# Performance work log

Measured on AMD Instinct MI355X. Metric: run time of the kernel, lower is better.

Reference implementation:

```python
import jax, jax.numpy as jnp
import numpy as np

L, H, P = 16384, 1024, 512
DT_MIN, DT_MAX = 1e-3, 1e-1
STEP_RESCALE = 1.0


def setup_inputs() -> dict:
    key = jax.random.key(0)
    ks = jax.random.split(key, 7)
    input_sequence = jax.random.normal(ks[0], (L, H), jnp.float32)
    # eigenvalues with negative real part (left half plane), HiPPO-like imag parts
    Lambda_re = -(jax.random.uniform(ks[1], (P,), jnp.float32) * 0.9 + 0.1)
    Lambda_im = jnp.pi * jnp.arange(P, dtype=jnp.float32)
    B = jax.random.normal(ks[2], (P, H, 2), jnp.float32) / jnp.sqrt(2.0 * H)   # real/imag of B_tilde (P,H)
    C = jax.random.normal(ks[3], (H, P, 2), jnp.float32) / jnp.sqrt(2.0 * P)   # real/imag of C_tilde (H,P)
    D = jax.random.normal(ks[4], (H,), jnp.float32)
    u01 = jax.random.uniform(ks[5], (P, 1), jnp.float32)
    log_step = jnp.log(DT_MIN) + u01 * (jnp.log(DT_MAX) - jnp.log(DT_MIN))     # (P,1)
    return dict(input_sequence=input_sequence, Lambda_re=Lambda_re, Lambda_im=Lambda_im,
                B=B, C=C, D=D, log_step=log_step)


def _binop(q_i, q_j):
    # diagonal linear recurrence composition: (A, b) pairs
    A_i, b_i = q_i
    A_j, b_j = q_j
    return A_j * A_i, A_j * b_i + b_j


def reference(input_sequence, Lambda_re, Lambda_im, B, C, D, log_step):
    Lambda = Lambda_re + 1j * Lambda_im                        # (P,) complex64
    B_tilde = B[..., 0] + 1j * B[..., 1]                       # (P,H)
    C_tilde = C[..., 0] + 1j * C[..., 1]                       # (H,P)
    step = STEP_RESCALE * jnp.exp(log_step[:, 0])              # (P,)
    # ZOH discretization
    Lambda_bar = jnp.exp(Lambda * step)                        # (P,)
    B_bar = ((Lambda_bar - 1.0) / Lambda)[:, None] * B_tilde   # (P,H)
    # Bu_elements: (L,P) complex
    Bu = input_sequence.astype(B_bar.dtype) @ B_bar.T
    Lambda_elems = jnp.broadcast_to(Lambda_bar, Bu.shape)      # (L,P)
    # parallel associative scan over the diagonal recurrence x_t = Lambda_bar*x_{t-1} + Bu_t
    _, xs = jax.lax.associative_scan(_binop, (Lambda_elems, Bu))
    ys = 2.0 * (xs @ C_tilde.T).real                           # conj_sym => factor 2, (L,H)
    return ys + D * input_sequence
```

## Files before the change

kernel.cpp:

```cpp
#include <hip/hip_runtime.h>
#include <math.h>

#define L_SEQ 16384
#define H_DIM 1024
#define P_DIM 512
#define N2P   1024
#define KDIM  1024
#define NKT   16
#define CHUNK 64
#define NCHUNK 256

typedef __attribute__((ext_vector_type(8))) short short8;
typedef __attribute__((ext_vector_type(4))) float f32x4;
typedef __attribute__((address_space(3))) const char* lds3_t;

__device__ __forceinline__ unsigned short f2bf(float f){
    unsigned int u = __float_as_uint(f);
    u = (u + 0x7FFFu + ((u >> 16) & 1u)) >> 16;
    return (unsigned short)u;
}
__device__ __forceinline__ float bf2f(unsigned int lo16){
    return __uint_as_float(lo16 << 16);
}

__global__ void k_prep_lambda(const float* __restrict__ lre, const float* __restrict__ lim,
                              const float* __restrict__ lstep,
                              float* __restrict__ lam, float* __restrict__ coef,
                              float* __restrict__ lpow)
{
    int p = threadIdx.x;
    double step = exp((double)lstep[p]);
    double dr = (double)lre[p], di = (double)lim[p];
    double ar = dr*step, ai = di*step;
    double er = exp(ar);
    double lbr = er*cos(ai), lbi = er*sin(ai);
    lam[2*p] = (float)lbr; lam[2*p+1] = (float)lbi;
    double nr = lbr - 1.0, ni = lbi;
    double d2 = dr*dr + di*di;
    coef[2*p]   = (float)((nr*dr + ni*di)/d2);
    coef[2*p+1] = (float)((ni*dr - nr*di)/d2);
    double xr = lbr, xi = lbi;
    #pragma unroll
    for (int s=0;s<6;s++){ double t = xr*xr - xi*xi; xi = 2.0*xr*xi; xr = t; }
    lpow[2*p] = (float)xr; lpow[2*p+1] = (float)xi;
}

__global__ __launch_bounds__(256)
void k_prep_BB(const float* __restrict__ B, const float* __restrict__ coef,
               unsigned short* __restrict__ BB)
{
    int i = blockIdx.x*256 + threadIdx.x;
    int p = i >> 10, h = i & 1023;
    float br = B[2*i], bi = B[2*i+1];
    float cr = coef[2*p], ci = coef[2*p+1];
    BB[(size_t)(2*p)*H_DIM + h]   = f2bf(cr*br - ci*bi);
    BB[(size_t)(2*p+1)*H_DIM + h] = f2bf(cr*bi + ci*br);
}

__global__ __launch_bounds__(256)
void k_prep_CC(const float* __restrict__ C, unsigned short* __restrict__ CC)
{
    int i = blockIdx.x*256 + threadIdx.x;
    int h = i >> 9, p = i & 511;
    float cr = C[2*i], ci = C[2*i+1];
    CC[(size_t)h*N2P + 2*p]     = f2bf(2.f*cr);
    CC[(size_t)h*N2P + 2*p + 1] = f2bf(-2.f*ci);
}

__global__ __launch_bounds__(256)
void k_cast(const float4* __restrict__ u, unsigned short* __restrict__ o)
{
    int i = blockIdx.x*256 + threadIdx.x;
    float4 a = u[2*i], b = u[2*i+1];
    union { short8 v; unsigned short s[8]; } r;
    r.s[0]=f2bf(a.x); r.s[1]=f2bf(a.y); r.s[2]=f2bf(a.z); r.s[3]=f2bf(a.w);
    r.s[4]=f2bf(b.x); r.s[5]=f2bf(b.y); r.s[6]=f2bf(b.z); r.s[7]=f2bf(b.w);
    *reinterpret_cast<short8*>(o + (size_t)i*8) = r.v;
}

template<int EPI>
__global__ __launch_bounds__(512, 2)
void gemm256(const unsigned short* __restrict__ A, const unsigned short* __restrict__ Bm,
             float* __restrict__ Cf, unsigned short* __restrict__ Cb,
             const float* __restrict__ Dv, const unsigned short* __restrict__ U16)
{
    __shared__ char lds[131072];
    const int tid  = threadIdx.x;
    const int lane = tid & 63;
    const int wid  = tid >> 6;
    const int wm = wid >> 2, wn = wid & 3;
    const int wg = ((int)blockIdx.x & 7) * 32 + ((int)blockIdx.x >> 3);
    const int tm = wg >> 2, tn = wg & 3;
    const int lr = lane & 15;

    const int scol = ((tid & 7) ^ ((tid >> 3) & 7)) << 3;
    const int srow = tid >> 3;
    const int kc0 = (((lane >> 4)      ^ (lr & 7)) << 4);
    const int kc1 = ((((lane >> 4) | 4) ^ (lr & 7)) << 4);
    const int aSub = wm*16384 + lr*128;
    const int bSub = 32768 + (wn >> 1)*16384 + (wn & 1)*8192 + lr*128;

#define GLOAD(SRC, DST) __builtin_amdgcn_global_load_lds( \
        (const __attribute__((address_space(1))) void*)(SRC), \
        (__attribute__((address_space(3))) void*)(DST), 16, 0, 0)
#define STAGE_A(kt_, h_) do{ \
    char* d_ = lds + (((kt_)&1)<<16) + (h_)*16384 + tid*16; \
    const unsigned short* s_ = A + (size_t)(tm*256 + (h_)*128 + srow)*KDIM + (size_t)(kt_)*64 + scol; \
    GLOAD(s_, d_); GLOAD(s_ + (size_t)64*KDIM, d_ + 8192); }while(0)
#define STAGE_B(kt_, h_) do{ \
    char* d_ = lds + (((kt_)&1)<<16) + 32768 + (h_)*16384 + tid*16; \
    const unsigned short* s_ = Bm + (size_t)(tn*256 + (h_)*128 + srow)*KDIM + (size_t)(kt_)*64 + scol; \
    GLOAD(s_, d_); GLOAD(s_ + (size_t)64*KDIM, d_ + 8192); }while(0)
#define DSR(D, P, IMM) asm volatile("ds_read_b128 %0, %1 offset:" IMM : "=v"(D) : "v"(P))
#define LGKM(N) do{ asm volatile("s_waitcnt lgkmcnt(" #N ")" ::: "memory"); \
                    __builtin_amdgcn_sched_barrier(0); }while(0)
#define VMC4  asm volatile("s_waitcnt vmcnt(4)" ::: "memory")
#define ABAR  asm volatile("s_barrier" ::: "memory")
#define SB0   __builtin_amdgcn_sched_barrier(0)
#define MFMA(a,b,c) __builtin_amdgcn_mfma_f32_16x16x32_bf16(a,b,c,0,0,0)
#define PRIO1 __builtin_amdgcn_s_setprio(1)
#define PRIO0 __builtin_amdgcn_s_setprio(0)

    short8 a1[4], a2[4], bb0[4], bb1[4];
    f32x4 acc[8][4];
    #pragma unroll
    for (int m=0;m<8;m++)
        #pragma unroll
        for (int n=0;n<4;n++) acc[m][n] = (f32x4){0.f,0.f,0.f,0.f};

    STAGE_A(0,0); STAGE_A(0,1); STAGE_B(0,0); STAGE_B(0,1); STAGE_B(1,0); STAGE_B(1,1);
    VMC4; ABAR;

    #pragma unroll 2
    for (int kt = 0; kt < NKT; ++kt) {
        const int sb = (kt & 1) << 16;
        const int tA = (kt+1 < NKT) ? kt+1 : NKT-1;
        const int tB = (kt+2 < NKT) ? kt+2 : NKT-1;
        lds3_t pa0 = (lds3_t)(lds + sb + aSub + kc0);
        lds3_t pa1 = (lds3_t)(lds + sb + aSub + kc1);
        lds3_t pb0 = (lds3_t)(lds + sb + bSub + kc0);
        lds3_t pb1 = (lds3_t)(lds + sb + bSub + kc1);

        DSR(a1[0], pa0, "0");    DSR(a1[1], pa0, "2048");
        DSR(a1[2], pa0, "4096"); DSR(a1[3], pa0, "6144");
        DSR(bb0[0], pb0, "0");    DSR(bb0[1], pb0, "2048");
        DSR(bb0[2], pb0, "4096"); DSR(bb0[3], pb0, "6144");
        STAGE_A(tA, 0); STAGE_A(tA, 1);
        DSR(a2[0], pa0, "8192");  DSR(a2[1], pa0, "10240");
        DSR(a2[2], pa0, "12288"); DSR(a2[3], pa0, "14336");
        LGKM(4);
        PRIO1;
        #pragma unroll
        for (int m=0;m<4;m++)
            #pragma unroll
            for (int n=0;n<4;n++) acc[m][n] = MFMA(a1[m], bb0[n], acc[m][n]);
        PRIO0; SB0;
        DSR(a1[0], pa1, "0");    DSR(a1[1], pa1, "2048");
        DSR(a1[2], pa1, "4096"); DSR(a1[3], pa1, "6144");
        DSR(bb1[0], pb1, "0");    DSR(bb1[1], pb1, "2048");
        DSR(bb1[2], pb1, "4096"); DSR(bb1[3], pb1, "6144");
        LGKM(8);
        PRIO1;
        #pragma unroll
        for (int m=0;m<4;m++)
            #pragma unroll
            for (int n=0;n<4;n++) acc[4+m][n] = MFMA(a2[m], bb0[n], acc[4+m][n]);
        PRIO0; SB0;
        DSR(a2[0], pa1, "8192");  DSR(a2[1], pa1, "10240");
        DSR(a2[2], pa1, "12288"); DSR(a2[3], pa1, "14336");
        LGKM(4);
        ABAR;
        STAGE_B(tB, 0); STAGE_B(tB, 1);
        PRIO1;
        #pragma unroll
        for (int m=0;m<4;m++)
            #pragma unroll
            for (int n=0;n<4;n++) acc[m][n] = MFMA(a1[m], bb1[n], acc[m][n]);
        PRIO0; SB0;
        LGKM(0);
        PRIO1;
        #pragma unroll
        for (int m=0;m<4;m++)
            #pragma unroll
            for (int n=0;n<4;n++) acc[4+m][n] = MFMA(a2[m], bb1[n], acc[4+m][n]);
        PRIO0; SB0;
        VMC4;
        ABAR;
    }
    asm volatile("s_waitcnt vmcnt(0)" ::: "memory");

    const int orow0 = tm*256 + wm*128 + (lane>>4)*4;
    const int ocol0 = tn*256 + wn*64 + lr;
    #pragma unroll
    for (int m=0;m<8;m++){
        #pragma unroll
        for (int n=0;n<4;n++){
            int row = orow0 + m*16, col = ocol0 + n*16;
            #pragma unroll
            for (int j=0;j<4;j++){
                size_t idx = (size_t)(row + j)*N2P + col;
                if (EPI) Cf[idx] = acc[m][n][j] + Dv[col]*bf2f(U16[idx]);
                else     Cb[idx] = f2bf(acc[m][n][j]);
            }
        }
    }
#undef GLOAD
#undef STAGE_A
#undef STAGE_B
#undef DSR
#undef LGKM
#undef VMC4
#undef ABAR
#undef SB0
#undef MFMA
#undef PRIO1
#undef PRIO0
}

__global__ __launch_bounds__(512)
void k_agg(const unsigned int* __restrict__ Bu, const float* __restrict__ lam,
           float* __restrict__ agg)
{
    int p = threadIdx.x, c = blockIdx.x;
    float lrr = lam[2*p], lii = lam[2*p+1];
    float xr = 0.f, xi = 0.f;
    const unsigned int* b2 = Bu + (size_t)c*CHUNK*512 + p;
    #pragma unroll 4
    for (int t=0;t<CHUNK;t++){
        unsigned int b = b2[(size_t)t*512];
        float br = __uint_as_float(b << 16);
        float bi = __uint_as_float(b & 0xffff0000u);
        float tr = lrr*xr - lii*xi + br;
        xi = lrr*xi + lii*xr + bi;
        xr = tr;
    }
    agg[((size_t)c*P_DIM + p)*2]     = xr;
    agg[((size_t)c*P_DIM + p)*2 + 1] = xi;
}

__global__ __launch_bounds__(256)
void k_scan(const float* __restrict__ agg, const float* __restrict__ lpow,
            float* __restrict__ xinit)
{
    __shared__ float sr[NCHUNK], si[NCHUNK];
    int c = threadIdx.x, p = blockIdx.x;
    float xr = agg[((size_t)c*P_DIM + p)*2];
    float xi = agg[((size_t)c*P_DIM + p)*2 + 1];
    sr[c] = xr; si[c] = xi;
    float wr = lpow[2*p], wi = lpow[2*p+1];
    for (int s=1; s<NCHUNK; s<<=1){
        __syncthreads();
        float ur = 0.f, ui = 0.f;
        if (c >= s){ ur = sr[c-s]; ui = si[c-s]; }
        __syncthreads();
        xr += wr*ur - wi*ui;
        xi += wr*ui + wi*ur;
        sr[c] = xr; si[c] = xi;
        float t = wr*wr - wi*wi; wi = 2.f*wr*wi; wr = t;
    }
    __syncthreads();
    float er = 0.f, ei = 0.f;
    if (c > 0){ er = sr[c-1]; ei = si[c-1]; }
    xinit[((size_t)c*P_DIM + p)*2]     = er;
    xinit[((size_t)c*P_DIM + p)*2 + 1] = ei;
}

__global__ __launch_bounds__(512)
void k_apply(const unsigned int* __restrict__ Bu, const float* __restrict__ lam,
             const float* __restrict__ xinit, unsigned int* __restrict__ xs)
{
    int p = threadIdx.x, c = blockIdx.x;
    float lrr = lam[2*p], lii = lam[2*p+1];
    float xr = xinit[((size_t)c*P_DIM + p)*2];
    float xi = xinit[((size_t)c*P_DIM + p)*2 + 1];
    const unsigned int* b2 = Bu + (size_t)c*CHUNK*512 + p;
    unsigned int* o = xs + (size_t)c*CHUNK*512 + p;
    #pragma unroll 4
    for (int t=0;t<CHUNK;t++){
        unsigned int b = b2[(size_t)t*512];
        float br = __uint_as_float(b << 16);
        float bi = __uint_as_float(b & 0xffff0000u);
        float tr = lrr*xr - lii*xi + br;
        xi = lrr*xi + lii*xr + bi;
        xr = tr;
        o[(size_t)t*512] = (unsigned int)f2bf(xr) | ((unsigned int)f2bf(xi) << 16);
    }
}

extern "C" void kernel_launch(void* const* d_in, const int* in_sizes, int n_in,
                              void* d_out, int out_size, void* d_ws, size_t ws_size,
                              hipStream_t stream)
{
    const float* u   = (const float*)d_in[0];
    const float* lre = (const float*)d_in[1];
    const float* lim = (const float*)d_in[2];
    const float* B   = (const float*)d_in[3];
    const float* C   = (const float*)d_in[4];
    const float* D   = (const float*)d_in[5];
    const float* ls  = (const float*)d_in[6];
    float* out = (float*)d_out;

    char* w = (char*)d_ws;
    unsigned short* u16  = (unsigned short*)(w + 0);
    unsigned short* xs16 = (unsigned short*)(w + 33554432);
    unsigned short* Bu16 = (unsigned short*)(w + 67108864);
    unsigned short* BB   = (unsigned short*)(w + 100663296);
    unsigned short* CC   = (unsigned short*)(w + 102760448);
    float* lam   = (float*)(w + 104857600);
    float* coef  = (float*)(w + 104861696);
    float* lpow  = (float*)(w + 104865792);
    float* agg   = (float*)(w + 104869888);
    float* xinit = (float*)(w + 105918464);

    k_prep_lambda<<<1, P_DIM, 0, stream>>>(lre, lim, ls, lam, coef, lpow);
    k_prep_BB<<<(P_DIM*H_DIM)/256, 256, 0, stream>>>(B, coef, BB);
    k_prep_CC<<<(H_DIM*P_DIM)/256, 256, 0, stream>>>(C, CC);
    k_cast<<<(L_SEQ*H_DIM)/(256*8), 256, 0, stream>>>((const float4*)u, u16);

    gemm256<0><<<256, 512, 0, stream>>>(u16, BB, nullptr, Bu16, nullptr, nullptr);

    k_agg<<<NCHUNK, P_DIM, 0, stream>>>((const unsigned int*)Bu16, lam, agg);
    k_scan<<<P_DIM, NCHUNK, 0, stream>>>(agg, lpow, xinit);
    k_apply<<<NCHUNK, P_DIM, 0, stream>>>((const unsigned int*)Bu16, lam, xinit,
                                          (unsigned int*)xs16);

    gemm256<1><<<256, 512, 0, stream>>>(xs16, CC, out, nullptr, D, u16);
}
```

Measured before the change: 129.0 us.

## Replace hand-scheduled asm GEMM main loop with simple compiler-scheduled double buffer

The bf16 MFMA GEMM main loop drops its hand-written ds_read_b128 asm, explicit lgkmcnt waits, sched barriers and s_setprio. It also drops the staggered prefetch in which the next A tile and the B tile two steps ahead were staged mid-iteration. Now A and B for the next k-tile are both issued at the top of each iteration, fragments are read with plain LDS loads, and each iteration ends with a full vmcnt(0) wait and a barrier. The code is simpler and leaves scheduling to the compiler, but it gives up the fine-grained overlap of LDS reads, global-to-LDS copies and MFMA issue, and adds a full memory drain each iteration.

```diff
diff --git a/kernel.cpp b/kernel.cpp
--- a/kernel.cpp
+++ b/kernel.cpp
@@ -12,7 +12,6 @@
 
 typedef __attribute__((ext_vector_type(8))) short short8;
 typedef __attribute__((ext_vector_type(4))) float f32x4;
-typedef __attribute__((address_space(3))) const char* lds3_t;
 
 __device__ __forceinline__ unsigned short f2bf(float f){
     unsigned int u = __float_as_uint(f);
@@ -111,83 +110,47 @@
     char* d_ = lds + (((kt_)&1)<<16) + 32768 + (h_)*16384 + tid*16; \
     const unsigned short* s_ = Bm + (size_t)(tn*256 + (h_)*128 + srow)*KDIM + (size_t)(kt_)*64 + scol; \
     GLOAD(s_, d_); GLOAD(s_ + (size_t)64*KDIM, d_ + 8192); }while(0)
-#define DSR(D, P, IMM) asm volatile("ds_read_b128 %0, %1 offset:" IMM : "=v"(D) : "v"(P))
-#define LGKM(N) do{ asm volatile("s_waitcnt lgkmcnt(" #N ")" ::: "memory"); \
-                    __builtin_amdgcn_sched_barrier(0); }while(0)
-#define VMC4  asm volatile("s_waitcnt vmcnt(4)" ::: "memory")
+#define RD(OFF) (*(const short8*)(lds + (OFF)))
+#define MFMA(a,b,c) __builtin_amdgcn_mfma_f32_16x16x32_bf16(a,b,c,0,0,0)
+#define VMC0  asm volatile("s_waitcnt vmcnt(0)" ::: "memory")
 #define ABAR  asm volatile("s_barrier" ::: "memory")
-#define SB0   __builtin_amdgcn_sched_barrier(0)
-#define MFMA(a,b,c) __builtin_amdgcn_mfma_f32_16x16x32_bf16(a,b,c,0,0,0)
-#define PRIO1 __builtin_amdgcn_s_setprio(1)
-#define PRIO0 __builtin_amdgcn_s_setprio(0)
-
-    short8 a1[4], a2[4], bb0[4], bb1[4];
+
     f32x4 acc[8][4];
     #pragma unroll
     for (int m=0;m<8;m++)
         #pragma unroll
         for (int n=0;n<4;n++) acc[m][n] = (f32x4){0.f,0.f,0.f,0.f};
 
-    STAGE_A(0,0); STAGE_A(0,1); STAGE_B(0,0); STAGE_B(0,1); STAGE_B(1,0); STAGE_B(1,1);
-    VMC4; ABAR;
+    STAGE_A(0,0); STAGE_A(0,1); STAGE_B(0,0); STAGE_B(0,1);
+    VMC0; ABAR;
 
     #pragma unroll 2
     for (int kt = 0; kt < NKT; ++kt) {
         const int sb = (kt & 1) << 16;
-        const int tA = (kt+1 < NKT) ? kt+1 : NKT-1;
-        const int tB = (kt+2 < NKT) ? kt+2 : NKT-1;
-        lds3_t pa0 = (lds3_t)(lds + sb + aSub + kc0);
-        lds3_t pa1 = (lds3_t)(lds + sb + aSub + kc1);
-        lds3_t pb0 = (lds3_t)(lds + sb + bSub + kc0);
-        lds3_t pb1 = (lds3_t)(lds + sb + bSub + kc1);
-
-        DSR(a1[0], pa0, "0");    DSR(a1[1], pa0, "2048");
-        DSR(a1[2], pa0, "4096"); DSR(a1[3], pa0, "6144");
-        DSR(bb0[0], pb0, "0");    DSR(bb0[1], pb0, "2048");
-        DSR(bb0[2], pb0, "4096"); DSR(bb0[3], pb0, "6144");
-        STAGE_A(tA, 0); STAGE_A(tA, 1);
-        DSR(a2[0], pa0, "8192");  DSR(a2[1], pa0, "10240");
-        DSR(a2[2], pa0, "12288"); DSR(a2[3], pa0, "14336");
-        LGKM(4);
-        PRIO1;
+        const int tN = (kt+1 < NKT) ? kt+1 : NKT-1;
+        STAGE_A(tN, 0); STAGE_A(tN, 1); STAGE_B(tN, 0); STAGE_B(tN, 1);
+
         #pragma unroll
-        for (int m=0;m<4;m++)
+        for (int ks=0; ks<2; ++ks){
+            const int kc = ks ? kc1 : kc0;
+            short8 bfr[4];
             #pragma unroll
-            for (int n=0;n<4;n++) acc[m][n] = MFMA(a1[m], bb0[n], acc[m][n]);
-        PRIO0; SB0;
-        DSR(a1[0], pa1, "0");    DSR(a1[1], pa1, "2048");
-        DSR(a1[2], pa1, "4096"); DSR(a1[3], pa1, "6144");
-        DSR(bb1[0], pb1, "0");    DSR(bb1[1], pb1, "2048");
-        DSR(bb1[2], pb1, "4096"); DSR(bb1[3], pb1, "6144");
-        LGKM(8);
-        PRIO1;
-        #pragma unroll
-        for (int m=0;m<4;m++)
+            for (int n=0;n<4;n++) bfr[n] = RD(sb + bSub + n*2048 + kc);
             #pragma unroll
-            for (int n=0;n<4;n++) acc[4+m][n] = MFMA(a2[m], bb0[n], acc[4+m][n]);
-        PRIO0; SB0;
-        DSR(a2[0], pa1, "8192");  DSR(a2[1], pa1, "10240");
-        DSR(a2[2], pa1, "12288"); DSR(a2[3], pa1, "14336");
-        LGKM(4);
+            for (int mh=0; mh<2; ++mh){
+                short8 afr[4];
+                #pragma unroll
+                for (int m=0;m<4;m++) afr[m] = RD(sb + aSub + (mh*4+m)*2048 + kc);
+                #pragma unroll
+                for (int m=0;m<4;m++)
+                    #pragma unroll
+                    for (int n=0;n<4;n++)
+                        acc[mh*4+m][n] = MFMA(afr[m], bfr[n], acc[mh*4+m][n]);
+            }
+        }
+        VMC0;
         ABAR;
-        STAGE_B(tB, 0); STAGE_B(tB, 1);
-        PRIO1;
-        #pragma unroll
-        for (int m=0;m<4;m++)
-            #pragma unroll
-            for (int n=0;n<4;n++) acc[m][n] = MFMA(a1[m], bb1[n], acc[m][n]);
-        PRIO0; SB0;
-        LGKM(0);
-        PRIO1;
-        #pragma unroll
-        for (int m=0;m<4;m++)
-            #pragma unroll
-            for (int n=0;n<4;n++) acc[4+m][n] = MFMA(a2[m], bb1[n], acc[4+m][n]);
-        PRIO0; SB0;
-        VMC4;
-        ABAR;
-    }
-    asm volatile("s_waitcnt vmcnt(0)" ::: "memory");
+    }
 
     const int orow0 = tm*256 + wm*128 + (lane>>4)*4;
     const int ocol0 = tn*256 + wn*64 + lr;
@@ -207,14 +170,10 @@
 #undef GLOAD
 #undef STAGE_A
 #undef STAGE_B
-#undef DSR
-#undef LGKM
-#undef VMC4
+#undef RD
+#undef MFMA
+#undef VMC0
 #undef ABAR
-#undef SB0
-#undef MFMA
-#undef PRIO1
-#undef PRIO0
 }
 
 __global__ __launch_bounds__(512)
```

Result: no change. 131.1 us (+1.6%).
